# Kernel tuning notes

Hardware: AMD Instinct MI355X
Metric: run time of the kernel (lower is better)

The kernel has to match this reference:

```python
import jax, jax.numpy as jnp
import numpy as np

B, N, E, H = 2, 256, 768, 12
D = E // H
LOG_2PI = float(np.log(2.0 * np.pi))


def setup_inputs() -> dict:
    key = jax.random.key(0)
    ks = jax.random.split(key, 8)
    return {
        "x": jax.random.normal(ks[0], (B, N, E), jnp.float32),
        "Wqkv": jax.random.normal(ks[1], (E, 3 * E), jnp.float32) * 0.02,
        "bqkv": jax.random.normal(ks[2], (3 * E,), jnp.float32) * 0.02,
        "Wproj": jax.random.normal(ks[3], (E, E), jnp.float32) * 0.02,
        "bproj": jax.random.normal(ks[4], (E,), jnp.float32) * 0.02,
        "mean": jax.random.normal(ks[5], (E, E), jnp.float32),
        "logvar": jax.random.normal(ks[6], (E, E), jnp.float32),
        "mix_coef": jax.random.normal(ks[7], (E,), jnp.float32),
    }


def reference(x, Wqkv, bqkv, Wproj, bproj, mean, logvar, mix_coef):
    b, n, e = x.shape
    # qkv projection; einops 'b n (h d qkv) -> qkv b h n d' (qkv is the INNERMOST split)
    qkv = (x @ Wqkv + bqkv).reshape(b, n, H, D, 3)
    qkv = jnp.transpose(qkv, (4, 0, 2, 1, 3))  # (3, b, h, n, d)
    q, k, v = qkv[0], qkv[1], qkv[2]

    # keys back to (b, n, e): 'b h n d -> b n (h d)'
    keys = jnp.transpose(k, (0, 2, 1, 3)).reshape(b, n, e)

    # MixtureSameFamily.log_prob: component Normal batch (E, E), mixture over last dim.
    # out[b,n,i] = logsumexp_j( log_softmax(mix_coef)[j] + logN(keys[b,n,i]; mean[i,j], std[i,j]) )
    log_mix = jax.nn.log_softmax(mix_coef)                      # (E,)
    std = jnp.exp(0.5 * logvar)                                  # (E, E)
    z = (keys[:, :, :, None] - mean[None, None, :, :]) / std     # (b, n, E, E)
    comp_lp = -0.5 * (z * z) - jnp.log(std) - 0.5 * LOG_2PI      # (b, n, E, E)
    key_mix = jax.nn.logsumexp(comp_lp + log_mix, axis=-1)       # (b, n, E)

    # 'b n (h d) -> b h n d'
    key_mix = jnp.transpose(key_mix.reshape(b, n, H, D), (0, 2, 1, 3))

    energy = jnp.einsum("bhqd,bhkd->bhqk", q, key_mix)
    att = jax.nn.softmax(energy, axis=-1) / jnp.sqrt(jnp.float32(e))
    out = jnp.einsum("bhql,bhld->bhqd", att, v)                  # (b, h, n, d)
    out = jnp.transpose(out, (0, 2, 1, 3)).reshape(b, n, e)
    return out @ Wproj + bproj
```

## Files before the change

kernel.cpp:

```cpp
#include <hip/hip_runtime.h>

#define LOG2E 1.4426950408889634f
#define LN2 0.6931471805599453f

typedef __attribute__((ext_vector_type(8))) short bf16x8;
typedef __attribute__((ext_vector_type(4))) float f32x4;

constexpr int Ee = 768;
constexpr int BN = 512;
constexpr long QC_OFF = 0;
constexpr long KT_OFF = 393216;
constexpr long VC_OFF = 786432;
constexpr long KM_OFF = 1179648;
constexpr long EN_OFF = 1572864;
constexpr long OA_OFF = 3145728;

__device__ __forceinline__ unsigned pk_hi(float x0, float x1) {
    return (__float_as_uint(x0) >> 16) | (__float_as_uint(x1) & 0xFFFF0000u);
}
__device__ __forceinline__ float rhi(float x) {
    return __uint_as_float(__float_as_uint(x) & 0xFFFF0000u);
}

template<int EPI>
__global__ __launch_bounds__(256)
void mfma_gemm(const float* __restrict__ A, int lda, long sAb, long sAh,
               const float* __restrict__ Bm, int ldb, long sBb, long sBh,
               float* __restrict__ C, int ldc, long sCb, long sCh,
               const float* __restrict__ bias, int K, int Hdiv,
               float* __restrict__ eq, float* __restrict__ ek,
               float* __restrict__ ev)
{
    __shared__ __align__(16) unsigned short sm[4 * 64 * 64];
    char* const smb = (char*)sm;
    const int tid = threadIdx.x;
    const int m0 = blockIdx.x * 64, n0 = blockIdx.y * 64;
    const int zb = blockIdx.z / Hdiv, zh = blockIdx.z - zb * Hdiv;
    A  += zb * sAb + zh * sAh;
    Bm += zb * sBb + zh * sBh;
    C  += zb * sCb + zh * sCh;

    const int lane = tid & 63, w = tid >> 6;
    const int wr = w >> 1, wc = w & 1;
    const int fr = lane & 15, fko2 = (lane >> 4) * 16;

    const bool isB = tid < 128;
    const int kq = isB ? (tid >> 4) : ((tid - 128) & 7);
    const int nq = tid & 15;
    const int mq = (tid - 128) >> 3;

    auto foff = [](int plane, int row, int cb) {
        return plane * 8192 + row * 128 + (cb ^ ((row & 7) << 4));
    };
    int wo[8];
    if (isB) {
        #pragma unroll
        for (int e = 0; e < 4; ++e) {
            wo[e]     = foff(2, nq * 4 + e, kq * 8);
            wo[e + 4] = foff(3, nq * 4 + e, kq * 8);
        }
    } else {
        #pragma unroll
        for (int r = 0; r < 4; ++r) {
            wo[r]     = foff(0, mq * 4 + r, kq * 8);
            wo[r + 4] = foff(1, mq * 4 + r, kq * 8);
        }
    }
    const int oA0h = foff(0, wr * 32 + fr,      fko2);
    const int oA1h = foff(0, wr * 32 + 16 + fr, fko2);
    const int oA0l = oA0h + 8192, oA1l = oA1h + 8192;
    const int oB0h = foff(2, wc * 32 + fr,      fko2);
    const int oB1h = foff(2, wc * 32 + 16 + fr, fko2);
    const int oB0l = oB0h + 8192, oB1l = oB1h + 8192;

    f32x4 acc00 = {}, acc01 = {}, acc10 = {}, acc11 = {};
    float4 r0, r1, r2, r3;

    auto load_regs = [&](int k0) {
        if (isB) {
            const float* p = &Bm[(long)(k0 + kq * 4) * ldb + n0 + nq * 4];
            r0 = *(const float4*)p; p += ldb;
            r1 = *(const float4*)p; p += ldb;
            r2 = *(const float4*)p; p += ldb;
            r3 = *(const float4*)p;
        } else {
            const float* p = &A[(long)(m0 + mq * 4) * lda + k0 + kq * 4];
            r0 = *(const float4*)p; p += lda;
            r1 = *(const float4*)p; p += lda;
            r2 = *(const float4*)p; p += lda;
            r3 = *(const float4*)p;
        }
    };

    auto cvt_store = [&](const float4& v, int o_hi, int o_lo) {
        uint2 hi; hi.x = pk_hi(v.x, v.y); hi.y = pk_hi(v.z, v.w);
        const float l0 = v.x - rhi(v.x), l1 = v.y - rhi(v.y);
        const float l2 = v.z - rhi(v.z), l3 = v.w - rhi(v.w);
        uint2 lo; lo.x = pk_hi(l0, l1); lo.y = pk_hi(l2, l3);
        *(uint2*)(smb + o_hi) = hi;
        *(uint2*)(smb + o_lo) = lo;
    };

    auto stage = [&]() {
        if (isB) {
            #pragma unroll
            for (int e = 0; e < 4; ++e) {
                float4 col;
                col.x = (&r0.x)[e]; col.y = (&r1.x)[e];
                col.z = (&r2.x)[e]; col.w = (&r3.x)[e];
                cvt_store(col, wo[e], wo[e + 4]);
            }
        } else {
            cvt_store(r0, wo[0], wo[4]);
            cvt_store(r1, wo[1], wo[5]);
            cvt_store(r2, wo[2], wo[6]);
            cvt_store(r3, wo[3], wo[7]);
        }
    };

    load_regs(0);
    for (int k0 = 0; k0 < K; k0 += 32) {
        __syncthreads();
        stage();
        __syncthreads();
        if (k0 + 32 < K) load_regs(k0 + 32);
        const bf16x8 Ah0 = *(const bf16x8*)(smb + oA0h);
        const bf16x8 Ah1 = *(const bf16x8*)(smb + oA1h);
        const bf16x8 Al0 = *(const bf16x8*)(smb + oA0l);
        const bf16x8 Al1 = *(const bf16x8*)(smb + oA1l);
        const bf16x8 Bh0 = *(const bf16x8*)(smb + oB0h);
        const bf16x8 Bh1 = *(const bf16x8*)(smb + oB1h);
        const bf16x8 Bl0 = *(const bf16x8*)(smb + oB0l);
        const bf16x8 Bl1 = *(const bf16x8*)(smb + oB1l);
        acc00 = __builtin_amdgcn_mfma_f32_16x16x32_bf16(Ah0, Bh0, acc00, 0, 0, 0);
        acc01 = __builtin_amdgcn_mfma_f32_16x16x32_bf16(Ah0, Bh1, acc01, 0, 0, 0);
        acc10 = __builtin_amdgcn_mfma_f32_16x16x32_bf16(Ah1, Bh0, acc10, 0, 0, 0);
        acc11 = __builtin_amdgcn_mfma_f32_16x16x32_bf16(Ah1, Bh1, acc11, 0, 0, 0);
        acc00 = __builtin_amdgcn_mfma_f32_16x16x32_bf16(Ah0, Bl0, acc00, 0, 0, 0);
        acc01 = __builtin_amdgcn_mfma_f32_16x16x32_bf16(Ah0, Bl1, acc01, 0, 0, 0);
        acc10 = __builtin_amdgcn_mfma_f32_16x16x32_bf16(Ah1, Bl0, acc10, 0, 0, 0);
        acc11 = __builtin_amdgcn_mfma_f32_16x16x32_bf16(Ah1, Bl1, acc11, 0, 0, 0);
        acc00 = __builtin_amdgcn_mfma_f32_16x16x32_bf16(Al0, Bh0, acc00, 0, 0, 0);
        acc01 = __builtin_amdgcn_mfma_f32_16x16x32_bf16(Al0, Bh1, acc01, 0, 0, 0);
        acc10 = __builtin_amdgcn_mfma_f32_16x16x32_bf16(Al1, Bh0, acc10, 0, 0, 0);
        acc11 = __builtin_amdgcn_mfma_f32_16x16x32_bf16(Al1, Bh1, acc11, 0, 0, 0);
    }

    const int rb = m0 + wr * 32 + (lane >> 4) * 4;
    const int cb = n0 + wc * 32 + fr;
    if (EPI == 1) {
        auto scat = [&](int row, int col, float x) {
            x += bias[col];
            const int i = col / 3, s = col - i * 3;
            if (s == 0)      eq[(long)row * Ee + i] = x;
            else if (s == 1) ek[(long)i * BN + row] = x;
            else             ev[(long)row * Ee + i] = x;
        };
        #pragma unroll
        for (int j = 0; j < 4; ++j) {
            scat(rb + j,      cb,      acc00[j]);
            scat(rb + j,      cb + 16, acc01[j]);
            scat(rb + j + 16, cb,      acc10[j]);
            scat(rb + j + 16, cb + 16, acc11[j]);
        }
    } else {
        const float b0  = bias ? bias[cb]      : 0.f;
        const float b16 = bias ? bias[cb + 16] : 0.f;
        #pragma unroll
        for (int j = 0; j < 4; ++j) C[(long)(rb + j +  0) * ldc + cb +  0] = acc00[j] + b0;
        #pragma unroll
        for (int j = 0; j < 4; ++j) C[(long)(rb + j +  0) * ldc + cb + 16] = acc01[j] + b16;
        #pragma unroll
        for (int j = 0; j < 4; ++j) C[(long)(rb + j + 16) * ldc + cb +  0] = acc10[j] + b0;
        #pragma unroll
        for (int j = 0; j < 4; ++j) C[(long)(rb + j + 16) * ldc + cb + 16] = acc11[j] + b16;
    }
}

__global__ __launch_bounds__(512)
void k_mixture(const float* __restrict__ mean, const float* __restrict__ logvar,
               const float* __restrict__ mix, const float* __restrict__ keysT,
               float* __restrict__ kmT)
{
    __shared__ __align__(16) float aS[768], bS[768], cS[768];
    __shared__ float sP[512][9];
    const int i = blockIdx.x;
    const int tid = threadIdx.x;

    for (int j = tid; j < 768; j += 512) {
        const float lv = logvar[i * Ee + j];
        const float mu = mean[i * Ee + j];
        const float istd2 = __builtin_amdgcn_exp2f(-lv * LOG2E);
        aS[j] = -0.5f * LOG2E * istd2;
        bS[j] = LOG2E * mu * istd2;
        cS[j] = fmaf(-0.5f * LOG2E * mu * mu, istd2, LOG2E * (mix[j] - 0.5f * lv));
    }
    __syncthreads();

    const int rg = tid & 63;
    const int jg = tid >> 6;
    float kv[8], k2[8], s[8];
    #pragma unroll
    for (int q = 0; q < 8; ++q) {
        kv[q] = keysT[(long)i * BN + q * 64 + rg];
        k2[q] = kv[q] * kv[q];
        s[q] = 0.f;
    }
    const float4* a4 = (const float4*)(aS + jg * 96);
    const float4* b4 = (const float4*)(bS + jg * 96);
    const float4* c4 = (const float4*)(cS + jg * 96);
    for (int it = 0; it < 24; ++it) {
        const float4 a = a4[it], b = b4[it], c = c4[it];
        #pragma unroll
        for (int q = 0; q < 8; ++q) {
            s[q] += __builtin_amdgcn_exp2f(fmaf(a.x, k2[q], fmaf(b.x, kv[q], c.x)));
            s[q] += __builtin_amdgcn_exp2f(fmaf(a.y, k2[q], fmaf(b.y, kv[q], c.y)));
            s[q] += __builtin_amdgcn_exp2f(fmaf(a.z, k2[q], fmaf(b.z, kv[q], c.z)));
            s[q] += __builtin_amdgcn_exp2f(fmaf(a.w, k2[q], fmaf(b.w, kv[q], c.w)));
        }
    }
    #pragma unroll
    for (int q = 0; q < 8; ++q)
        sP[q * 64 + rg][jg] = s[q];
    __syncthreads();

    const float* rp = sP[tid];
    const float t0 = ((rp[0] + rp[1]) + (rp[2] + rp[3]))
                   + ((rp[4] + rp[5]) + (rp[6] + rp[7]));
    kmT[(long)i * BN + tid] = LN2 * __builtin_amdgcn_logf(t0);
}

__global__ __launch_bounds__(256)
void k_softmax(float* __restrict__ e)
{
    const int row = blockIdx.x * 4 + (threadIdx.x >> 6);
    const int lane = threadIdx.x & 63;
    float4* p = (float4*)(e + (long)row * 256);
    float4 v = p[lane];
    float m = fmaxf(fmaxf(v.x, v.y), fmaxf(v.z, v.w));
    #pragma unroll
    for (int off = 32; off; off >>= 1) m = fmaxf(m, __shfl_xor(m, off, 64));
    v.x = __builtin_amdgcn_exp2f((v.x - m) * LOG2E);
    v.y = __builtin_amdgcn_exp2f((v.y - m) * LOG2E);
    v.z = __builtin_amdgcn_exp2f((v.z - m) * LOG2E);
    v.w = __builtin_amdgcn_exp2f((v.w - m) * LOG2E);
    float s = v.x + v.y + v.z + v.w;
    #pragma unroll
    for (int off = 32; off; off >>= 1) s += __shfl_xor(s, off, 64);
    const float sc = 1.0f / (s * 27.712812921102035f);
    v.x *= sc; v.y *= sc; v.z *= sc; v.w *= sc;
    p[lane] = v;
}

extern "C" void kernel_launch(void* const* d_in, const int* in_sizes, int n_in,
                              void* d_out, int out_size, void* d_ws, size_t ws_size,
                              hipStream_t stream)
{
    (void)in_sizes; (void)n_in; (void)out_size; (void)ws_size;
    const float* x      = (const float*)d_in[0];
    const float* Wqkv   = (const float*)d_in[1];
    const float* bqkv   = (const float*)d_in[2];
    const float* Wproj  = (const float*)d_in[3];
    const float* bproj  = (const float*)d_in[4];
    const float* mean   = (const float*)d_in[5];
    const float* logvar = (const float*)d_in[6];
    const float* mixc   = (const float*)d_in[7];
    float* out = (float*)d_out;
    float* ws = (float*)d_ws;
    float* qc     = ws + QC_OFF;
    float* keysT  = ws + KT_OFF;
    float* vc     = ws + VC_OFF;
    float* kmT    = ws + KM_OFF;
    float* energy = ws + EN_OFF;
    float* oat    = ws + OA_OFF;

    mfma_gemm<1><<<dim3(8,36,1),256,0,stream>>>(
        x,768,0,0, Wqkv,2304,0,0, nullptr,0,0,0, bqkv, 768, 1,
        qc, keysT, vc);
    k_mixture<<<768,512,0,stream>>>(mean, logvar, mixc, keysT, kmT);
    mfma_gemm<0><<<dim3(4,4,24),256,0,stream>>>(
        qc,768,196608,64, kmT,512,256,32768, energy,256,786432,65536,
        nullptr, 64, 12, nullptr,nullptr,nullptr);
    k_softmax<<<1536,256,0,stream>>>(energy);
    mfma_gemm<0><<<dim3(4,1,24),256,0,stream>>>(
        energy,256,786432,65536, vc,768,196608,64, oat,768,196608,64,
        nullptr, 256, 12, nullptr,nullptr,nullptr);
    mfma_gemm<0><<<dim3(8,12,1),256,0,stream>>>(
        oat,768,0,0, Wproj,768,0,0, out,768,0,0, bproj, 768, 1,
        nullptr,nullptr,nullptr);
}
```

Measured before the change: 109.3 us.

## Fuse softmax into attention-times-V kernel and pack mixture FMAs

Replaces the separate softmax kernel and the generic att@V GEMM with a single kernel. It loads a 64-row energy tile, computes the softmax in registers and writes split-bf16 (hi/lo) probabilities into swizzled LDS, then runs MFMA against V tiles staged through LDS. This removes one launch and a full write and re-read of the energy matrix. Separately, the mixture kernel's quadratic evaluation now uses packed v_pk_fma_f32 and v_pk_add_f32 inline asm to halve VALU instruction count in the exp-bound loop. The fused kernel uses only 96 blocks, and its single-buffered LDS loop with two barriers per step may limit overlap.

Result: faster. 102.5 us (-6.2%).

```diff
diff --git a/kernel.cpp b/kernel.cpp
--- a/kernel.cpp
+++ b/kernel.cpp
@@ -5,6 +5,7 @@
 
 typedef __attribute__((ext_vector_type(8))) short bf16x8;
 typedef __attribute__((ext_vector_type(4))) float f32x4;
+typedef __attribute__((ext_vector_type(2))) float f32x2;
 
 constexpr int Ee = 768;
 constexpr int BN = 512;
@@ -20,6 +21,16 @@
 }
 __device__ __forceinline__ float rhi(float x) {
     return __uint_as_float(__float_as_uint(x) & 0xFFFF0000u);
+}
+__device__ __forceinline__ f32x2 pk_fma2(f32x2 a, f32x2 b, f32x2 c) {
+    f32x2 d;
+    asm("v_pk_fma_f32 %0, %1, %2, %3" : "=v"(d) : "v"(a), "v"(b), "v"(c));
+    return d;
+}
+__device__ __forceinline__ f32x2 pk_add2(f32x2 a, f32x2 b) {
+    f32x2 d;
+    asm("v_pk_add_f32 %0, %1, %2" : "=v"(d) : "v"(a), "v"(b));
+    return d;
 }
 
 template<int EPI>
@@ -199,29 +210,36 @@
 
     const int rg = tid & 63;
     const int jg = tid >> 6;
-    float kv[8], k2[8], s[8];
+    f32x2 kvd[8], k2d[8], s2[8];
     #pragma unroll
     for (int q = 0; q < 8; ++q) {
-        kv[q] = keysT[(long)i * BN + q * 64 + rg];
-        k2[q] = kv[q] * kv[q];
-        s[q] = 0.f;
+        const float kv = keysT[(long)i * BN + q * 64 + rg];
+        const float k2 = kv * kv;
+        kvd[q] = (f32x2){kv, kv};
+        k2d[q] = (f32x2){k2, k2};
+        s2[q] = (f32x2){0.f, 0.f};
     }
     const float4* a4 = (const float4*)(aS + jg * 96);
     const float4* b4 = (const float4*)(bS + jg * 96);
     const float4* c4 = (const float4*)(cS + jg * 96);
     for (int it = 0; it < 24; ++it) {
         const float4 a = a4[it], b = b4[it], c = c4[it];
+        const f32x2 a01 = {a.x, a.y}, a23 = {a.z, a.w};
+        const f32x2 b01 = {b.x, b.y}, b23 = {b.z, b.w};
+        const f32x2 c01 = {c.x, c.y}, c23 = {c.z, c.w};
         #pragma unroll
         for (int q = 0; q < 8; ++q) {
-            s[q] += __builtin_amdgcn_exp2f(fmaf(a.x, k2[q], fmaf(b.x, kv[q], c.x)));
-            s[q] += __builtin_amdgcn_exp2f(fmaf(a.y, k2[q], fmaf(b.y, kv[q], c.y)));
-            s[q] += __builtin_amdgcn_exp2f(fmaf(a.z, k2[q], fmaf(b.z, kv[q], c.z)));
-            s[q] += __builtin_amdgcn_exp2f(fmaf(a.w, k2[q], fmaf(b.w, kv[q], c.w)));
+            f32x2 t0 = pk_fma2(a01, k2d[q], pk_fma2(b01, kvd[q], c01));
+            f32x2 t1 = pk_fma2(a23, k2d[q], pk_fma2(b23, kvd[q], c23));
+            f32x2 e0 = { __builtin_amdgcn_exp2f(t0.x), __builtin_amdgcn_exp2f(t0.y) };
+            f32x2 e1 = { __builtin_amdgcn_exp2f(t1.x), __builtin_amdgcn_exp2f(t1.y) };
+            s2[q] = pk_add2(s2[q], e0);
+            s2[q] = pk_add2(s2[q], e1);
         }
     }
     #pragma unroll
     for (int q = 0; q < 8; ++q)
-        sP[q * 64 + rg][jg] = s[q];
+        sP[q * 64 + rg][jg] = s2[q].x + s2[q].y;
     __syncthreads();
 
     const float* rp = sP[tid];
@@ -231,25 +249,149 @@
 }
 
 __global__ __launch_bounds__(256)
-void k_softmax(float* __restrict__ e)
+void k_smpv(const float* __restrict__ energy, const float* __restrict__ vc,
+            float* __restrict__ oat)
 {
-    const int row = blockIdx.x * 4 + (threadIdx.x >> 6);
-    const int lane = threadIdx.x & 63;
-    float4* p = (float4*)(e + (long)row * 256);
-    float4 v = p[lane];
-    float m = fmaxf(fmaxf(v.x, v.y), fmaxf(v.z, v.w));
-    #pragma unroll
-    for (int off = 32; off; off >>= 1) m = fmaxf(m, __shfl_xor(m, off, 64));
-    v.x = __builtin_amdgcn_exp2f((v.x - m) * LOG2E);
-    v.y = __builtin_amdgcn_exp2f((v.y - m) * LOG2E);
-    v.z = __builtin_amdgcn_exp2f((v.z - m) * LOG2E);
-    v.w = __builtin_amdgcn_exp2f((v.w - m) * LOG2E);
-    float s = v.x + v.y + v.z + v.w;
-    #pragma unroll
-    for (int off = 32; off; off >>= 1) s += __shfl_xor(s, off, 64);
-    const float sc = 1.0f / (s * 27.712812921102035f);
-    v.x *= sc; v.y *= sc; v.z *= sc; v.w *= sc;
-    p[lane] = v;
+    __shared__ __align__(16) unsigned short att[32768];
+    __shared__ __align__(16) unsigned short bv[8192];
+    char* const attb = (char*)att;
+    char* const bvb  = (char*)bv;
+    const int tid = threadIdx.x;
+    const int tile = blockIdx.x, bh = blockIdx.y;
+    const int b = bh / 12, h = bh - b * 12;
+    const float* E = energy + (long)bh * 65536 + (long)tile * 64 * 256;
+    const float* V = vc + (long)b * 196608 + h * 64;
+    float* O = oat + ((long)b * 256 + tile * 64) * 768 + h * 64;
+
+    const int w = tid >> 6, lane = tid & 63;
+
+    {
+        const int rl = w * 16 + (lane >> 2);
+        const int mq = (lane & 3) * 64;
+        float4 ev[16];
+        const float* erow = E + (long)rl * 256 + mq;
+        #pragma unroll
+        for (int t = 0; t < 16; ++t) ev[t] = *(const float4*)(erow + t * 4);
+        float mx = -__builtin_inff();
+        #pragma unroll
+        for (int t = 0; t < 16; ++t)
+            mx = fmaxf(mx, fmaxf(fmaxf(ev[t].x, ev[t].y), fmaxf(ev[t].z, ev[t].w)));
+        mx = fmaxf(mx, __shfl_xor(mx, 1, 64));
+        mx = fmaxf(mx, __shfl_xor(mx, 2, 64));
+        float sum = 0.f;
+        #pragma unroll
+        for (int t = 0; t < 16; ++t) {
+            ev[t].x = __builtin_amdgcn_exp2f((ev[t].x - mx) * LOG2E);
+            ev[t].y = __builtin_amdgcn_exp2f((ev[t].y - mx) * LOG2E);
+            ev[t].z = __builtin_amdgcn_exp2f((ev[t].z - mx) * LOG2E);
+            ev[t].w = __builtin_amdgcn_exp2f((ev[t].w - mx) * LOG2E);
+            sum += (ev[t].x + ev[t].y) + (ev[t].z + ev[t].w);
+        }
+        sum += __shfl_xor(sum, 1, 64);
+        sum += __shfl_xor(sum, 2, 64);
+        const float sc = 1.0f / (sum * 27.712812921102035f);
+        const int rxor = (rl & 7) << 4;
+        #pragma unroll
+        for (int t = 0; t < 16; ++t) {
+            const float x0 = ev[t].x * sc, x1 = ev[t].y * sc;
+            const float x2 = ev[t].z * sc, x3 = ev[t].w * sc;
+            uint2 hi; hi.x = pk_hi(x0, x1); hi.y = pk_hi(x2, x3);
+            const float l0 = x0 - rhi(x0), l1 = x1 - rhi(x1);
+            const float l2 = x2 - rhi(x2), l3 = x3 - rhi(x3);
+            uint2 lo; lo.x = pk_hi(l0, l1); lo.y = pk_hi(l2, l3);
+            const int cb = (mq + t * 4) * 2;
+            *(uint2*)(attb + (long)rl * 512 + (cb ^ rxor))         = hi;
+            *(uint2*)(attb + 32768 + (long)rl * 512 + (cb ^ rxor)) = lo;
+        }
+    }
+
+    const int wr = w >> 1, wc = w & 1;
+    const int fr = lane & 15, fko2 = (lane >> 4) * 16;
+    const int rA0 = wr * 32 + fr, rA1 = rA0 + 16;
+    const int rB0 = wc * 32 + fr, rB1 = rB0 + 16;
+    const int xA0 = (rA0 & 7) << 4, xA1 = (rA1 & 7) << 4;
+    const int oB0h = rB0 * 128 + (fko2 ^ ((rB0 & 7) << 4));
+    const int oB1h = rB1 * 128 + (fko2 ^ ((rB1 & 7) << 4));
+    const int oB0l = oB0h + 8192, oB1l = oB1h + 8192;
+
+    const bool isB = tid < 128;
+    const int kq = tid >> 4;
+    const int nq = tid & 15;
+    int wo[8];
+    #pragma unroll
+    for (int e = 0; e < 4; ++e) {
+        const int row = nq * 4 + e;
+        wo[e]     = row * 128 + ((kq * 8) ^ ((row & 7) << 4));
+        wo[e + 4] = wo[e] + 8192;
+    }
+
+    f32x4 acc00 = {}, acc01 = {}, acc10 = {}, acc11 = {};
+    float4 r0, r1, r2, r3;
+    auto load_regs = [&](int k0) {
+        if (isB) {
+            const float* p = &V[(long)(k0 + kq * 4) * 768 + nq * 4];
+            r0 = *(const float4*)p; p += 768;
+            r1 = *(const float4*)p; p += 768;
+            r2 = *(const float4*)p; p += 768;
+            r3 = *(const float4*)p;
+        }
+    };
+    auto cvt_store = [&](const float4& v, int o_hi, int o_lo) {
+        uint2 hi; hi.x = pk_hi(v.x, v.y); hi.y = pk_hi(v.z, v.w);
+        const float l0 = v.x - rhi(v.x), l1 = v.y - rhi(v.y);
+        const float l2 = v.z - rhi(v.z), l3 = v.w - rhi(v.w);
+        uint2 lo; lo.x = pk_hi(l0, l1); lo.y = pk_hi(l2, l3);
+        *(uint2*)(bvb + o_hi) = hi;
+        *(uint2*)(bvb + o_lo) = lo;
+    };
+
+    load_regs(0);
+    for (int k0 = 0; k0 < 256; k0 += 32) {
+        __syncthreads();
+        if (isB) {
+            #pragma unroll
+            for (int e = 0; e < 4; ++e) {
+                float4 col;
+                col.x = (&r0.x)[e]; col.y = (&r1.x)[e];
+                col.z = (&r2.x)[e]; col.w = (&r3.x)[e];
+                cvt_store(col, wo[e], wo[e + 4]);
+            }
+        }
+        __syncthreads();
+        if (k0 + 32 < 256) load_regs(k0 + 32);
+        const int cA = k0 * 2 + fko2;
+        const bf16x8 Ah0 = *(const bf16x8*)(attb + (long)rA0 * 512 + (cA ^ xA0));
+        const bf16x8 Ah1 = *(const bf16x8*)(attb + (long)rA1 * 512 + (cA ^ xA1));
+        const bf16x8 Al0 = *(const bf16x8*)(attb + 32768 + (long)rA0 * 512 + (cA ^ xA0));
+        const bf16x8 Al1 = *(const bf16x8*)(attb + 32768 + (long)rA1 * 512 + (cA ^ xA1));
+        const bf16x8 Bh0 = *(const bf16x8*)(bvb + oB0h);
+        const bf16x8 Bh1 = *(const bf16x8*)(bvb + oB1h);
+        const bf16x8 Bl0 = *(const bf16x8*)(bvb + oB0l);
+        const bf16x8 Bl1 = *(const bf16x8*)(bvb + oB1l);
+        acc00 = __builtin_amdgcn_mfma_f32_16x16x32_bf16(Ah0, Bh0, acc00, 0, 0, 0);
+        acc01 = __builtin_amdgcn_mfma_f32_16x16x32_bf16(Ah0, Bh1, acc01, 0, 0, 0);
+        acc10 = __builtin_amdgcn_mfma_f32_16x16x32_bf16(Ah1, Bh0, acc10, 0, 0, 0);
+        acc11 = __builtin_amdgcn_mfma_f32_16x16x32_bf16(Ah1, Bh1, acc11, 0, 0, 0);
+        acc00 = __builtin_amdgcn_mfma_f32_16x16x32_bf16(Ah0, Bl0, acc00, 0, 0, 0);
+        acc01 = __builtin_amdgcn_mfma_f32_16x16x32_bf16(Ah0, Bl1, acc01, 0, 0, 0);
+        acc10 = __builtin_amdgcn_mfma_f32_16x16x32_bf16(Ah1, Bl0, acc10, 0, 0, 0);
+        acc11 = __builtin_amdgcn_mfma_f32_16x16x32_bf16(Ah1, Bl1, acc11, 0, 0, 0);
+        acc00 = __builtin_amdgcn_mfma_f32_16x16x32_bf16(Al0, Bh0, acc00, 0, 0, 0);
+        acc01 = __builtin_amdgcn_mfma_f32_16x16x32_bf16(Al0, Bh1, acc01, 0, 0, 0);
+        acc10 = __builtin_amdgcn_mfma_f32_16x16x32_bf16(Al1, Bh0, acc10, 0, 0, 0);
+        acc11 = __builtin_amdgcn_mfma_f32_16x16x32_bf16(Al1, Bh1, acc11, 0, 0, 0);
+    }
+
+    const int rb = wr * 32 + (lane >> 4) * 4;
+    const int cb = wc * 32 + fr;
+    #pragma unroll
+    for (int j = 0; j < 4; ++j) O[(long)(rb + j +  0) * 768 + cb +  0] = acc00[j];
+    #pragma unroll
+    for (int j = 0; j < 4; ++j) O[(long)(rb + j +  0) * 768 + cb + 16] = acc01[j];
+    #pragma unroll
+    for (int j = 0; j < 4; ++j) O[(long)(rb + j + 16) * 768 + cb +  0] = acc10[j];
+    #pragma unroll
+    for (int j = 0; j < 4; ++j) O[(long)(rb + j + 16) * 768 + cb + 16] = acc11[j];
 }
 
 extern "C" void kernel_launch(void* const* d_in, const int* in_sizes, int n_in,
@@ -281,10 +423,7 @@
     mfma_gemm<0><<<dim3(4,4,24),256,0,stream>>>(
         qc,768,196608,64, kmT,512,256,32768, energy,256,786432,65536,
         nullptr, 64, 12, nullptr,nullptr,nullptr);
-    k_softmax<<<1536,256,0,stream>>>(energy);
-    mfma_gemm<0><<<dim3(4,1,24),256,0,stream>>>(
-        energy,256,786432,65536, vc,768,196608,64, oat,768,196608,64,
-        nullptr, 256, 12, nullptr,nullptr,nullptr);
+    k_smpv<<<dim3(4,24,1),256,0,stream>>>(energy, vc, oat);
     mfma_gemm<0><<<dim3(8,12,1),256,0,stream>>>(
         oat,768,0,0, Wproj,768,0,0, out,768,0,0, bproj, 768, 1,
         nullptr,nullptr,nullptr);
```
